# Kernel optimization log

Measured on AMD Instinct MI355X. Metric: run time of the kernel, lower is better.

The kernel has to match this reference:

```python
import jax, jax.numpy as jnp
import numpy as np
from math import sqrt

# dims
B, H, P, N, D = 4, 8, 32, 32, 16   # batch, heads, n_patches, channels, patch_len
L = P * N                           # 1024 token positions
SEQ, PRED, WIN, E, NF = 512, 96, 10, 2, 6  # seq_len, pred_len, attention_window, e_layers, n_fore
EPS = float(np.finfo(np.float32).eps)      # torch RMSNorm default eps (finfo eps)


def setup_inputs() -> dict:
    key = jax.random.key(0)
    ks = jax.random.split(key, 8)
    return dict(
        tokens=jax.random.normal(ks[0], (B, H, L, D), jnp.float32),
        x_original=jax.random.normal(ks[1], (B, SEQ, N), jnp.float32),
        log_scales=jnp.full((E,), np.log(2.0), jnp.float32),
        attn_norm_w=jnp.ones((E, D), jnp.float32),
        conv_up_w=jax.random.normal(ks[2], (E, 2 * H, 1, 3), jnp.float32) * 0.1,
        conv_down_w=jax.random.normal(ks[3], (E, H, 2, 1), jnp.float32) * 0.1,
        ffn_norm_w=jnp.ones((E, D), jnp.float32),
        mix_w=jax.random.normal(ks[4], (1, H), jnp.float32) * 0.3,
        mix_b=jnp.zeros((1,), jnp.float32),
        fore_w=jax.random.normal(ks[5], (NF, P), jnp.float32) * 0.1,
        fore_b=jnp.zeros((NF,), jnp.float32),
    )


def _rms(x, w):
    # torch.nn.RMSNorm over last dim (patch_len)
    return x * jax.lax.rsqrt(jnp.mean(x * x, axis=-1, keepdims=True) + EPS) * w


def _mask():
    # pid repeated per-channel; True entries are masked out
    pid = jnp.repeat(jnp.arange(P), N)
    diff = pid[None, :] - pid[:, None]  # pid[key] - pid[query]
    return (diff <= 0) | (diff >= WIN)  # [L, L]


def _signed_attn(h, log_scale, mask):
    # scores: [B,H,L,L]; A = softmax(+s) - softmax(-s) with banded mask
    scores = jnp.einsum('bhld,bhmd->bhlm', h, h)
    scale = jnp.clip(jnp.exp(log_scale), 1.0, 30.0) / sqrt(D)
    pos = jnp.where(mask, -10000.0, scores)
    neg = jnp.where(mask, -10000.0, -scores)
    A = jax.nn.softmax(scale * pos, axis=-1) - jax.nn.softmax(scale * neg, axis=-1)
    return jnp.einsum('bhlm,bhmd->bhld', A, h)


def _conv_ffn(x, up_w, down_w, norm_w):
    # depthwise causal conv along patch time dim D; x: [B,H,L,D]
    r = x.transpose(0, 2, 1, 3).reshape(B * L, H, D)
    r = jnp.pad(r, ((0, 0), (0, 0), (2, 0)))  # causal left-pad (kernel_size-1)
    dn = ('NCH', 'OIH', 'NCH')
    r = jax.lax.conv_general_dilated(r, up_w, (1,), 'VALID', dimension_numbers=dn, feature_group_count=H)
    r = jax.nn.gelu(r, approximate=False)
    r = jax.lax.conv_general_dilated(r, down_w, (1,), 'VALID', dimension_numbers=dn, feature_group_count=H)
    r = r.reshape(B, L, H, D).transpose(0, 2, 1, 3)
    return _rms(x + r, norm_w)


def reference(tokens, x_original, log_scales, attn_norm_w, conv_up_w, conv_down_w,
              ffn_norm_w, mix_w, mix_b, fore_w, fore_b):
    mask = _mask()
    h = tokens
    for l in range(E):
        h = _rms(h + _signed_attn(h, log_scales[l], mask), attn_norm_w[l])
        h = _conv_ffn(h, conv_up_w[l], conv_down_w[l], ffn_norm_w[l])
    # aggregate heads -> forecast
    h = h.reshape(B, H, P, N, D).transpose(0, 3, 4, 2, 1)       # (B,N,D,P,H)
    h = jnp.einsum('bndph,h->bndp', h, mix_w[0]) + mix_b[0]      # channel_mixing
    f = jnp.einsum('bndp,fp->bndf', h, fore_w) + fore_b          # fore_projection
    f = f.reshape(B, N, D * NF)[:, :, -PRED:]                    # flatten + tail slice
    forecast = f.transpose(0, 2, 1)                              # (B,pred_len,N)
    return forecast, x_original
```

## Files before the change

kernel.cpp:

```cpp
#include <hip/hip_runtime.h>
#include <hip/hip_bf16.h>
#include <math.h>

#define BB 4
#define HH 8
#define PP 32
#define NN 32
#define DD 16
#define LL 1024
#define WINW 10
#define NFF 6
#define PREDL 96
#define SEQL 512
#define EPSF 1.1920928955078125e-07f
#define KROW 24
#define KTS 296
#define PROW 40
#define XROW 20

typedef __attribute__((ext_vector_type(8))) short bf16x8;
typedef __attribute__((ext_vector_type(4))) float f32x4;

__device__ __forceinline__ unsigned cvtpk(float a, float b) {
    unsigned r;
    asm("v_cvt_pk_bf16_f32 %0, %1, %2" : "=v"(r) : "v"(a), "v"(b));
    return r;
}
__device__ __forceinline__ unsigned long long pk64(unsigned lo, unsigned hi) {
    return (unsigned long long)lo | ((unsigned long long)hi << 32);
}

template <int MODE>
__device__ __forceinline__ void layer_body(
    const float* __restrict__ hin, float* __restrict__ hout,
    const float* __restrict__ log_scales, const float* __restrict__ attn_norm,
    const float* __restrict__ up_w, const float* __restrict__ down_w,
    const float* __restrict__ ffn_norm, int layer, int blk, int tid,
    short* hK, short* VT, short (*Pp)[16 * PROW], short (*Pn)[16 * PROW],
    float* xls, float (*comb)[64][8], float (*combl)[2][16],
    const float* __restrict__ mix_w, const float* __restrict__ mix_b,
    const float* __restrict__ fore_w, const float* __restrict__ fore_b,
    float* __restrict__ out)
{
    int bh  = blk >> 5;
    int hh  = bh & 7;
    int p0  = blk & 31;
    int nstage = min(9, (PP - 1) - p0);

    int wid  = tid >> 6;
    int qh   = wid >> 1;
    int ch   = wid & 1;
    int lane = tid & 63;
    int quad = lane >> 4, n16 = lane & 15;

    {
        const float4* src = (const float4*)(hin + ((size_t)bh * LL + (p0 + 1) * NN) * DD);
        int nf4 = nstage * 128;
        #pragma unroll
        for (int k = 0; k < 5; ++k) {
            int i = tid + k * 256;
            if (i < nf4) {
                int row = i >> 2, j = i & 3;
                float4 v = src[i];
                unsigned pk0 = cvtpk(v.x, v.y);
                unsigned pk1 = cvtpk(v.z, v.w);
                *(unsigned long long*)&hK[row * KROW + j * 4] = pk64(pk0, pk1);
                int d0 = j * 4;
                VT[(d0 + 0) * KTS + row] = (short)(pk0 & 0xffff);
                VT[(d0 + 1) * KTS + row] = (short)(pk0 >> 16);
                VT[(d0 + 2) * KTS + row] = (short)(pk1 & 0xffff);
                VT[(d0 + 3) * KTS + row] = (short)(pk1 >> 16);
            }
        }
    }

    bf16x8 Aq;
    #pragma unroll
    for (int j = 0; j < 8; ++j) Aq[j] = 0;
    if (quad < 2) {
        const float4* qp4 = (const float4*)(hin +
            ((size_t)bh * LL + p0 * NN + qh * 16 + n16) * DD + quad * 8);
        float4 a = qp4[0], b = qp4[1];
        union { bf16x8 v; unsigned u[4]; } uu;
        uu.u[0] = cvtpk(a.x, a.y);
        uu.u[1] = cvtpk(a.z, a.w);
        uu.u[2] = cvtpk(b.x, b.y);
        uu.u[3] = cvtpk(b.z, b.w);
        Aq = uu.v;
    }
    float rs[4] = {0.f, 0.f, 0.f, 0.f};
    if (ch == 0) {
        #pragma unroll
        for (int r = 0; r < 4; ++r)
            rs[r] = hin[((size_t)bh * LL + p0 * NN + qh * 16 + quad * 4 + r) * DD + n16];
    }

    float sc  = fminf(fmaxf(__expf(log_scales[layer]), 1.0f), 30.0f) * 0.25f;
    float sc2 = sc * 1.4426950408889634f;

    __syncthreads();

    f32x4 Op, On;
    Op[0] = Op[1] = Op[2] = Op[3] = 0.f;
    On[0] = On[1] = On[2] = On[3] = 0.f;
    float lpp = 0.f, lnn = 0.f;
    short* myPp = Pp[wid];
    short* myPn = Pn[wid];

    int c0 = ch ? 4 : 0;
    int c1 = ch ? nstage : min(4, nstage);

    for (int c = c0; c < c1; ++c) {
        int kb = c * 32;
        #pragma unroll
        for (int kt = 0; kt < 2; ++kt) {
            bf16x8 Bk;
            #pragma unroll
            for (int j = 0; j < 8; ++j) Bk[j] = 0;
            if (quad < 2)
                Bk = *(const bf16x8*)&hK[(kb + kt * 16 + n16) * KROW + quad * 8];
            f32x4 z; z[0] = z[1] = z[2] = z[3] = 0.f;
            f32x4 S = __builtin_amdgcn_mfma_f32_16x16x32_bf16(Bk, Aq, z, 0, 0, 0);
            float ep[4], en[4];
            #pragma unroll
            for (int r = 0; r < 4; ++r) {
                float t = sc2 * S[r];
                ep[r] = exp2f(t);
                en[r] = exp2f(-t);
                lpp += ep[r]; lnn += en[r];
            }
            *(unsigned long long*)&myPp[n16 * PROW + kt * 16 + quad * 4] =
                pk64(cvtpk(ep[0], ep[1]), cvtpk(ep[2], ep[3]));
            *(unsigned long long*)&myPn[n16 * PROW + kt * 16 + quad * 4] =
                pk64(cvtpk(en[0], en[1]), cvtpk(en[2], en[3]));
        }
        bf16x8 Bv = *(const bf16x8*)&VT[n16 * KTS + kb + quad * 8];
        bf16x8 Ap = *(const bf16x8*)&myPp[n16 * PROW + quad * 8];
        bf16x8 An = *(const bf16x8*)&myPn[n16 * PROW + quad * 8];
        Op = __builtin_amdgcn_mfma_f32_16x16x32_bf16(Ap, Bv, Op, 0, 0, 0);
        On = __builtin_amdgcn_mfma_f32_16x16x32_bf16(An, Bv, On, 0, 0, 0);
    }

    lpp += __shfl_xor(lpp, 16); lpp += __shfl_xor(lpp, 32);
    lnn += __shfl_xor(lnn, 16); lnn += __shfl_xor(lnn, 32);

    if (ch == 1) {
        *(f32x4*)&comb[qh][lane][0] = Op;
        *(f32x4*)&comb[qh][lane][4] = On;
        if (lane < 16) {
            combl[qh][0][lane] = lpp;
            combl[qh][1][lane] = lnn;
        }
    }
    __syncthreads();
    if (ch == 1) return;

    {
        f32x4 o2 = *(const f32x4*)&comb[qh][lane][0];
        f32x4 n2 = *(const f32x4*)&comb[qh][lane][4];
        #pragma unroll
        for (int r = 0; r < 4; ++r) { Op[r] += o2[r]; On[r] += n2[r]; }
        lpp += combl[qh][0][n16];
        lnn += combl[qh][1][n16];
    }

    float lpr[4], lnr[4];
    #pragma unroll
    for (int r = 0; r < 4; ++r) {
        lpr[r] = __shfl(lpp, quad * 4 + r);
        lnr[r] = __shfl(lnn, quad * 4 + r);
    }

    #pragma unroll
    for (int r = 0; r < 4; ++r) {
        float lp = lpr[r], ln = lnr[r];
        float rl = (lp > 0.f) ? (1.0f / lp) : 0.f;
        float rn = (ln > 0.f) ? (1.0f / ln) : 0.f;
        float v  = rs[r] + Op[r] * rl - On[r] * rn;
        float ss = v * v;
        ss += __shfl_xor(ss, 1); ss += __shfl_xor(ss, 2);
        ss += __shfl_xor(ss, 4); ss += __shfl_xor(ss, 8);
        float rr = rsqrtf(ss * (1.0f / 16.0f) + EPSF);
        xls[(qh * 16 + quad * 4 + r) * XROW + n16] = v * rr * attn_norm[layer * DD + n16];
    }

    {
        int q = qh * 16 + n16;
        int g = quad;

        const float* uw = up_w + (size_t)(layer * 2 * HH + 2 * hh) * 3;
        float w00 = uw[0], w01 = uw[1], w02 = uw[2];
        float w10 = uw[3], w11 = uw[4], w12 = uw[5];
        const float* dw = down_w + (size_t)(layer * HH + hh) * 2;
        float dc0 = dw[0], dc1 = dw[1];

        float xm2 = g ? xls[q * XROW + 4 * g - 2] : 0.f;
        float xm1 = g ? xls[q * XROW + 4 * g - 1] : 0.f;
        float4 xv = *(const float4*)&xls[q * XROW + 4 * g];
        float xa[6] = {xm2, xm1, xv.x, xv.y, xv.z, xv.w};

        float v4[4], ss = 0.f;
        #pragma unroll
        for (int i = 0; i < 4; ++i) {
            float u0 = w00 * xa[i] + w01 * xa[i + 1] + w02 * xa[i + 2];
            float u1 = w10 * xa[i] + w11 * xa[i + 1] + w12 * xa[i + 2];
            float g0 = 0.5f * u0 * (1.0f + erff(u0 * 0.7071067811865475f));
            float g1 = 0.5f * u1 * (1.0f + erff(u1 * 0.7071067811865475f));
            float vv = xa[i] * 0.f + xa[i + 2] + dc0 * g0 + dc1 * g1;
            v4[i] = vv; ss += vv * vv;
        }
        ss += __shfl_xor(ss, 16); ss += __shfl_xor(ss, 32);
        float r2 = rsqrtf(ss * (1.0f / 16.0f) + EPSF);

        const float4 fn = *(const float4*)&ffn_norm[layer * DD + 4 * g];
        float vals[4];
        vals[0] = v4[0] * r2 * fn.x;
        vals[1] = v4[1] * r2 * fn.y;
        vals[2] = v4[2] * r2 * fn.z;
        vals[3] = v4[3] * r2 * fn.w;

        if (MODE == 0) {
            float* op = hout + ((size_t)bh * LL + p0 * NN + q) * DD + 4 * g;
            *(float4*)op = *(float4*)vals;
        } else {
            int b2 = bh >> 3;
            float mwh = mix_w[hh];
            bool isc = (hh == 0) && (p0 == 0);
            float mbv = mix_b[0];
            #pragma unroll
            for (int fi = 0; fi < NFF; ++fi) {
                float cst = 0.f;
                if (isc) {
                    float s = 0.f;
                    for (int p = 0; p < PP; ++p) s += fore_w[fi * PP + p];
                    cst = fore_b[fi] + mbv * s;
                }
                float c = mwh * fore_w[fi * PP + p0];
                #pragma unroll
                for (int i = 0; i < 4; ++i)
                    atomicAdd(&out[((size_t)(b2 * DD + 4 * g + i) * NFF + fi) * NN + q],
                              c * vals[i] + cst);
            }
        }
    }
}

__global__ __launch_bounds__(256) void layer0_kernel(
    const float* __restrict__ tokens, float* __restrict__ hA,
    const float* __restrict__ log_scales, const float* __restrict__ attn_norm,
    const float* __restrict__ up_w, const float* __restrict__ down_w,
    const float* __restrict__ ffn_norm,
    const float* __restrict__ x_orig, float* __restrict__ out)
{
    __shared__ short hK[9 * 32 * KROW];
    __shared__ short VT[16 * KTS];
    __shared__ short Pp[4][16 * PROW];
    __shared__ short Pn[4][16 * PROW];
    __shared__ float xls[32 * XROW];
    __shared__ float comb[2][64][8];
    __shared__ float combl[2][2][16];

    int blk = blockIdx.x;
    int tid = threadIdx.x;

    if (tid < 3) {
        float4 z; z.x = z.y = z.z = z.w = 0.f;
        ((float4*)out)[blk * 3 + tid] = z;
    }
    if (tid < 16) {
        const float4* x4 = (const float4*)x_orig;
        float4* o4 = (float4*)(out + BB * PREDL * NN);
        o4[blk * 16 + tid] = x4[blk * 16 + tid];
    }

    layer_body<0>(tokens, hA, log_scales, attn_norm, up_w, down_w, ffn_norm, 0,
                  blk, tid, hK, VT, Pp, Pn, xls, comb, combl,
                  nullptr, nullptr, nullptr, nullptr, nullptr);
}

__global__ __launch_bounds__(256) void layer1_kernel(
    const float* __restrict__ hA,
    const float* __restrict__ log_scales, const float* __restrict__ attn_norm,
    const float* __restrict__ up_w, const float* __restrict__ down_w,
    const float* __restrict__ ffn_norm,
    const float* __restrict__ mix_w, const float* __restrict__ mix_b,
    const float* __restrict__ fore_w, const float* __restrict__ fore_b,
    float* __restrict__ out)
{
    __shared__ short hK[9 * 32 * KROW];
    __shared__ short VT[16 * KTS];
    __shared__ short Pp[4][16 * PROW];
    __shared__ short Pn[4][16 * PROW];
    __shared__ float xls[32 * XROW];
    __shared__ float comb[2][64][8];
    __shared__ float combl[2][2][16];

    int blk = blockIdx.x;
    int tid = threadIdx.x;

    layer_body<1>(hA, nullptr, log_scales, attn_norm, up_w, down_w, ffn_norm, 1,
                  blk, tid, hK, VT, Pp, Pn, xls, comb, combl,
                  mix_w, mix_b, fore_w, fore_b, out);
}

static int find_by_size(const int* s, int n, int want, int occurrence) {
    int seen = 0;
    for (int i = 0; i < n; ++i)
        if (s[i] == want) { if (seen == occurrence) return i; ++seen; }
    return -1;
}

extern "C" void kernel_launch(void* const* d_in, const int* in_sizes, int n_in,
                              void* d_out, int out_size, void* d_ws, size_t ws_size,
                              hipStream_t stream) {
    int it  = find_by_size(in_sizes, n_in, 524288, 0);
    int ix  = find_by_size(in_sizes, n_in, 65536, 0);
    int ils = find_by_size(in_sizes, n_in, 2, 0);
    int ian = find_by_size(in_sizes, n_in, 32, 0);
    int icu = find_by_size(in_sizes, n_in, 96, 0);
    int icd = find_by_size(in_sizes, n_in, 32, 1);
    int ifn = find_by_size(in_sizes, n_in, 32, 2);
    int imw = find_by_size(in_sizes, n_in, 8, 0);
    int imb = find_by_size(in_sizes, n_in, 1, 0);
    int ifw = find_by_size(in_sizes, n_in, 192, 0);
    int ifb = find_by_size(in_sizes, n_in, 6, 0);
    if (it < 0 || ix < 0 || ils < 0 || ian < 0 || icu < 0 || icd < 0 ||
        ifn < 0 || imw < 0 || imb < 0 || ifw < 0 || ifb < 0) {
        it = 0; ix = 1; ils = 2; ian = 3; icu = 4; icd = 5; ifn = 6;
        imw = 7; imb = 8; ifw = 9; ifb = 10;
    }

    const float* tokens     = (const float*)d_in[it];
    const float* x_orig     = (const float*)d_in[ix];
    const float* log_scales = (const float*)d_in[ils];
    const float* attn_norm  = (const float*)d_in[ian];
    const float* up_w       = (const float*)d_in[icu];
    const float* down_w     = (const float*)d_in[icd];
    const float* ffn_norm   = (const float*)d_in[ifn];
    const float* mix_w      = (const float*)d_in[imw];
    const float* mix_b      = (const float*)d_in[imb];
    const float* fore_w     = (const float*)d_in[ifw];
    const float* fore_b     = (const float*)d_in[ifb];
    float* out = (float*)d_out;

    float* hA = (float*)d_ws;

    layer0_kernel<<<1024, 256, 0, stream>>>(tokens, hA, log_scales, attn_norm,
                                            up_w, down_w, ffn_norm, x_orig, out);
    layer1_kernel<<<1024, 256, 0, stream>>>(hA, log_scales, attn_norm,
                                            up_w, down_w, ffn_norm,
                                            mix_w, mix_b, fore_w, fore_b, out);
}
```

Baseline: 109.7 us.

## Fuse both encoder layers into one kernel with halo recomputation in LDS

After: 120.0 us. 9.4% more time.

```diff
diff --git a/kernel.cpp b/kernel.cpp
--- a/kernel.cpp
+++ b/kernel.cpp
@@ -8,13 +8,13 @@
 #define NN 32
 #define DD 16
 #define LL 1024
-#define WINW 10
 #define NFF 6
 #define PREDL 96
 #define SEQL 512
 #define EPSF 1.1920928955078125e-07f
 #define KROW 24
-#define KTS 296
+#define KTS0 680
+#define H1ROW 20
 #define PROW 40
 #define XROW 20
 
@@ -30,277 +30,361 @@
     return (unsigned long long)lo | ((unsigned long long)hi << 32);
 }
 
-template <int MODE>
-__device__ __forceinline__ void layer_body(
-    const float* __restrict__ hin, float* __restrict__ hout,
-    const float* __restrict__ log_scales, const float* __restrict__ attn_norm,
-    const float* __restrict__ up_w, const float* __restrict__ down_w,
-    const float* __restrict__ ffn_norm, int layer, int blk, int tid,
-    short* hK, short* VT, short (*Pp)[16 * PROW], short (*Pn)[16 * PROW],
-    float* xls, float (*comb)[64][8], float (*combl)[2][16],
-    const float* __restrict__ mix_w, const float* __restrict__ mix_b,
-    const float* __restrict__ fore_w, const float* __restrict__ fore_b,
-    float* __restrict__ out)
+__global__ __launch_bounds__(256) void prep_kernel(float* __restrict__ out)
 {
-    int bh  = blk >> 5;
-    int hh  = bh & 7;
-    int p0  = blk & 31;
-    int nstage = min(9, (PP - 1) - p0);
-
-    int wid  = tid >> 6;
-    int qh   = wid >> 1;
-    int ch   = wid & 1;
-    int lane = tid & 63;
-    int quad = lane >> 4, n16 = lane & 15;
-
-    {
-        const float4* src = (const float4*)(hin + ((size_t)bh * LL + (p0 + 1) * NN) * DD);
-        int nf4 = nstage * 128;
-        #pragma unroll
-        for (int k = 0; k < 5; ++k) {
-            int i = tid + k * 256;
-            if (i < nf4) {
-                int row = i >> 2, j = i & 3;
-                float4 v = src[i];
-                unsigned pk0 = cvtpk(v.x, v.y);
-                unsigned pk1 = cvtpk(v.z, v.w);
-                *(unsigned long long*)&hK[row * KROW + j * 4] = pk64(pk0, pk1);
-                int d0 = j * 4;
-                VT[(d0 + 0) * KTS + row] = (short)(pk0 & 0xffff);
-                VT[(d0 + 1) * KTS + row] = (short)(pk0 >> 16);
-                VT[(d0 + 2) * KTS + row] = (short)(pk1 & 0xffff);
-                VT[(d0 + 3) * KTS + row] = (short)(pk1 >> 16);
-            }
-        }
-    }
-
-    bf16x8 Aq;
-    #pragma unroll
-    for (int j = 0; j < 8; ++j) Aq[j] = 0;
-    if (quad < 2) {
-        const float4* qp4 = (const float4*)(hin +
-            ((size_t)bh * LL + p0 * NN + qh * 16 + n16) * DD + quad * 8);
-        float4 a = qp4[0], b = qp4[1];
-        union { bf16x8 v; unsigned u[4]; } uu;
-        uu.u[0] = cvtpk(a.x, a.y);
-        uu.u[1] = cvtpk(a.z, a.w);
-        uu.u[2] = cvtpk(b.x, b.y);
-        uu.u[3] = cvtpk(b.z, b.w);
-        Aq = uu.v;
-    }
-    float rs[4] = {0.f, 0.f, 0.f, 0.f};
-    if (ch == 0) {
-        #pragma unroll
-        for (int r = 0; r < 4; ++r)
-            rs[r] = hin[((size_t)bh * LL + p0 * NN + qh * 16 + quad * 4 + r) * DD + n16];
-    }
-
-    float sc  = fminf(fmaxf(__expf(log_scales[layer]), 1.0f), 30.0f) * 0.25f;
-    float sc2 = sc * 1.4426950408889634f;
-
-    __syncthreads();
-
-    f32x4 Op, On;
-    Op[0] = Op[1] = Op[2] = Op[3] = 0.f;
-    On[0] = On[1] = On[2] = On[3] = 0.f;
-    float lpp = 0.f, lnn = 0.f;
-    short* myPp = Pp[wid];
-    short* myPn = Pn[wid];
-
-    int c0 = ch ? 4 : 0;
-    int c1 = ch ? nstage : min(4, nstage);
-
-    for (int c = c0; c < c1; ++c) {
-        int kb = c * 32;
-        #pragma unroll
-        for (int kt = 0; kt < 2; ++kt) {
-            bf16x8 Bk;
-            #pragma unroll
-            for (int j = 0; j < 8; ++j) Bk[j] = 0;
-            if (quad < 2)
-                Bk = *(const bf16x8*)&hK[(kb + kt * 16 + n16) * KROW + quad * 8];
-            f32x4 z; z[0] = z[1] = z[2] = z[3] = 0.f;
-            f32x4 S = __builtin_amdgcn_mfma_f32_16x16x32_bf16(Bk, Aq, z, 0, 0, 0);
-            float ep[4], en[4];
-            #pragma unroll
-            for (int r = 0; r < 4; ++r) {
-                float t = sc2 * S[r];
-                ep[r] = exp2f(t);
-                en[r] = exp2f(-t);
-                lpp += ep[r]; lnn += en[r];
-            }
-            *(unsigned long long*)&myPp[n16 * PROW + kt * 16 + quad * 4] =
-                pk64(cvtpk(ep[0], ep[1]), cvtpk(ep[2], ep[3]));
-            *(unsigned long long*)&myPn[n16 * PROW + kt * 16 + quad * 4] =
-                pk64(cvtpk(en[0], en[1]), cvtpk(en[2], en[3]));
-        }
-        bf16x8 Bv = *(const bf16x8*)&VT[n16 * KTS + kb + quad * 8];
-        bf16x8 Ap = *(const bf16x8*)&myPp[n16 * PROW + quad * 8];
-        bf16x8 An = *(const bf16x8*)&myPn[n16 * PROW + quad * 8];
-        Op = __builtin_amdgcn_mfma_f32_16x16x32_bf16(Ap, Bv, Op, 0, 0, 0);
-        On = __builtin_amdgcn_mfma_f32_16x16x32_bf16(An, Bv, On, 0, 0, 0);
-    }
-
-    lpp += __shfl_xor(lpp, 16); lpp += __shfl_xor(lpp, 32);
-    lnn += __shfl_xor(lnn, 16); lnn += __shfl_xor(lnn, 32);
-
-    if (ch == 1) {
-        *(f32x4*)&comb[qh][lane][0] = Op;
-        *(f32x4*)&comb[qh][lane][4] = On;
-        if (lane < 16) {
-            combl[qh][0][lane] = lpp;
-            combl[qh][1][lane] = lnn;
-        }
-    }
-    __syncthreads();
-    if (ch == 1) return;
-
-    {
-        f32x4 o2 = *(const f32x4*)&comb[qh][lane][0];
-        f32x4 n2 = *(const f32x4*)&comb[qh][lane][4];
-        #pragma unroll
-        for (int r = 0; r < 4; ++r) { Op[r] += o2[r]; On[r] += n2[r]; }
-        lpp += combl[qh][0][n16];
-        lnn += combl[qh][1][n16];
-    }
-
-    float lpr[4], lnr[4];
-    #pragma unroll
-    for (int r = 0; r < 4; ++r) {
-        lpr[r] = __shfl(lpp, quad * 4 + r);
-        lnr[r] = __shfl(lnn, quad * 4 + r);
-    }
-
-    #pragma unroll
-    for (int r = 0; r < 4; ++r) {
-        float lp = lpr[r], ln = lnr[r];
-        float rl = (lp > 0.f) ? (1.0f / lp) : 0.f;
-        float rn = (ln > 0.f) ? (1.0f / ln) : 0.f;
-        float v  = rs[r] + Op[r] * rl - On[r] * rn;
-        float ss = v * v;
-        ss += __shfl_xor(ss, 1); ss += __shfl_xor(ss, 2);
-        ss += __shfl_xor(ss, 4); ss += __shfl_xor(ss, 8);
-        float rr = rsqrtf(ss * (1.0f / 16.0f) + EPSF);
-        xls[(qh * 16 + quad * 4 + r) * XROW + n16] = v * rr * attn_norm[layer * DD + n16];
-    }
-
-    {
-        int q = qh * 16 + n16;
-        int g = quad;
-
-        const float* uw = up_w + (size_t)(layer * 2 * HH + 2 * hh) * 3;
-        float w00 = uw[0], w01 = uw[1], w02 = uw[2];
-        float w10 = uw[3], w11 = uw[4], w12 = uw[5];
-        const float* dw = down_w + (size_t)(layer * HH + hh) * 2;
-        float dc0 = dw[0], dc1 = dw[1];
-
-        float xm2 = g ? xls[q * XROW + 4 * g - 2] : 0.f;
-        float xm1 = g ? xls[q * XROW + 4 * g - 1] : 0.f;
-        float4 xv = *(const float4*)&xls[q * XROW + 4 * g];
-        float xa[6] = {xm2, xm1, xv.x, xv.y, xv.z, xv.w};
-
-        float v4[4], ss = 0.f;
-        #pragma unroll
-        for (int i = 0; i < 4; ++i) {
-            float u0 = w00 * xa[i] + w01 * xa[i + 1] + w02 * xa[i + 2];
-            float u1 = w10 * xa[i] + w11 * xa[i + 1] + w12 * xa[i + 2];
-            float g0 = 0.5f * u0 * (1.0f + erff(u0 * 0.7071067811865475f));
-            float g1 = 0.5f * u1 * (1.0f + erff(u1 * 0.7071067811865475f));
-            float vv = xa[i] * 0.f + xa[i + 2] + dc0 * g0 + dc1 * g1;
-            v4[i] = vv; ss += vv * vv;
-        }
-        ss += __shfl_xor(ss, 16); ss += __shfl_xor(ss, 32);
-        float r2 = rsqrtf(ss * (1.0f / 16.0f) + EPSF);
-
-        const float4 fn = *(const float4*)&ffn_norm[layer * DD + 4 * g];
-        float vals[4];
-        vals[0] = v4[0] * r2 * fn.x;
-        vals[1] = v4[1] * r2 * fn.y;
-        vals[2] = v4[2] * r2 * fn.z;
-        vals[3] = v4[3] * r2 * fn.w;
-
-        if (MODE == 0) {
-            float* op = hout + ((size_t)bh * LL + p0 * NN + q) * DD + 4 * g;
-            *(float4*)op = *(float4*)vals;
-        } else {
-            int b2 = bh >> 3;
-            float mwh = mix_w[hh];
-            bool isc = (hh == 0) && (p0 == 0);
-            float mbv = mix_b[0];
-            #pragma unroll
-            for (int fi = 0; fi < NFF; ++fi) {
-                float cst = 0.f;
-                if (isc) {
-                    float s = 0.f;
-                    for (int p = 0; p < PP; ++p) s += fore_w[fi * PP + p];
-                    cst = fore_b[fi] + mbv * s;
-                }
-                float c = mwh * fore_w[fi * PP + p0];
-                #pragma unroll
-                for (int i = 0; i < 4; ++i)
-                    atomicAdd(&out[((size_t)(b2 * DD + 4 * g + i) * NFF + fi) * NN + q],
-                              c * vals[i] + cst);
-            }
-        }
-    }
-}
-
-__global__ __launch_bounds__(256) void layer0_kernel(
-    const float* __restrict__ tokens, float* __restrict__ hA,
-    const float* __restrict__ log_scales, const float* __restrict__ attn_norm,
-    const float* __restrict__ up_w, const float* __restrict__ down_w,
-    const float* __restrict__ ffn_norm,
-    const float* __restrict__ x_orig, float* __restrict__ out)
-{
-    __shared__ short hK[9 * 32 * KROW];
-    __shared__ short VT[16 * KTS];
-    __shared__ short Pp[4][16 * PROW];
-    __shared__ short Pn[4][16 * PROW];
-    __shared__ float xls[32 * XROW];
-    __shared__ float comb[2][64][8];
-    __shared__ float combl[2][2][16];
-
-    int blk = blockIdx.x;
-    int tid = threadIdx.x;
-
-    if (tid < 3) {
+    int t = blockIdx.x * 256 + threadIdx.x;
+    if (t < BB * DD * NFF * NN / 4) {
         float4 z; z.x = z.y = z.z = z.w = 0.f;
-        ((float4*)out)[blk * 3 + tid] = z;
-    }
-    if (tid < 16) {
-        const float4* x4 = (const float4*)x_orig;
-        float4* o4 = (float4*)(out + BB * PREDL * NN);
-        o4[blk * 16 + tid] = x4[blk * 16 + tid];
-    }
-
-    layer_body<0>(tokens, hA, log_scales, attn_norm, up_w, down_w, ffn_norm, 0,
-                  blk, tid, hK, VT, Pp, Pn, xls, comb, combl,
-                  nullptr, nullptr, nullptr, nullptr, nullptr);
-}
-
-__global__ __launch_bounds__(256) void layer1_kernel(
-    const float* __restrict__ hA,
+        ((float4*)out)[t] = z;
+    }
+}
+
+__global__ __launch_bounds__(512) void mega_kernel(
+    const float* __restrict__ tokens,
     const float* __restrict__ log_scales, const float* __restrict__ attn_norm,
     const float* __restrict__ up_w, const float* __restrict__ down_w,
     const float* __restrict__ ffn_norm,
     const float* __restrict__ mix_w, const float* __restrict__ mix_b,
     const float* __restrict__ fore_w, const float* __restrict__ fore_b,
-    float* __restrict__ out)
+    const float* __restrict__ x_orig, float* __restrict__ out)
 {
-    __shared__ short hK[9 * 32 * KROW];
-    __shared__ short VT[16 * KTS];
-    __shared__ short Pp[4][16 * PROW];
-    __shared__ short Pn[4][16 * PROW];
-    __shared__ float xls[32 * XROW];
-    __shared__ float comb[2][64][8];
-    __shared__ float combl[2][2][16];
+    __shared__ short hK0[672 * KROW];
+    __shared__ short VT0[16 * KTS0];
+    __shared__ float h1[13 * 32 * H1ROW];
+    __shared__ short Pp[8][16 * PROW];
+    __shared__ short Pn[8][16 * PROW];
+    __shared__ float xls[8][16 * XROW];
 
     int blk = blockIdx.x;
-    int tid = threadIdx.x;
-
-    layer_body<1>(hA, nullptr, log_scales, attn_norm, up_w, down_w, ffn_norm, 1,
-                  blk, tid, hK, VT, Pp, Pn, xls, comb, combl,
-                  mix_w, mix_b, fore_w, fore_b, out);
+    int bh  = blk >> 3;
+    int hh  = bh & 7;
+    int ri  = blk & 7;
+    int a   = ri * 4;
+    int lo0 = a;
+    int hi0 = min(32, a + 13);
+    int P0  = hi0 - lo0;
+    int klo = lo0 + 1;
+    int khi = min(32, hi0 + 9);
+    int KP0 = khi - klo;
+
+    int tid  = threadIdx.x;
+    int wid  = tid >> 6;
+    int lane = tid & 63;
+    int quad = lane >> 4, n16 = lane & 15;
+
+    if (tid < 64) {
+        const float4* x4 = (const float4*)x_orig;
+        float4* o4 = (float4*)(out + BB * PREDL * NN);
+        o4[blk * 64 + tid] = x4[blk * 64 + tid];
+    }
+
+    {
+        const float4* src = (const float4*)(tokens + ((size_t)bh * LL + klo * NN) * DD);
+        int nf4 = KP0 * 128;
+        for (int i = tid; i < nf4; i += 512) {
+            int row = i >> 2, j = i & 3;
+            float4 v = src[i];
+            unsigned pk0 = cvtpk(v.x, v.y);
+            unsigned pk1 = cvtpk(v.z, v.w);
+            *(unsigned long long*)&hK0[row * KROW + j * 4] = pk64(pk0, pk1);
+            int d0 = j * 4;
+            VT0[(d0 + 0) * KTS0 + row] = (short)(pk0 & 0xffff);
+            VT0[(d0 + 1) * KTS0 + row] = (short)(pk0 >> 16);
+            VT0[(d0 + 2) * KTS0 + row] = (short)(pk1 & 0xffff);
+            VT0[(d0 + 3) * KTS0 + row] = (short)(pk1 >> 16);
+        }
+    }
+
+    float sc0 = fminf(fmaxf(__expf(log_scales[0]), 1.0f), 30.0f)
+                * 0.25f * 1.4426950408889634f;
+    float sc1 = fminf(fmaxf(__expf(log_scales[1]), 1.0f), 30.0f)
+                * 0.25f * 1.4426950408889634f;
+
+    short* myPp = Pp[wid];
+    short* myPn = Pn[wid];
+    float* myxls = xls[wid];
+
+    __syncthreads();
+
+    {
+        int ntask = P0 * 2;
+        for (int t = wid; t < ntask; t += 8) {
+            int pi = t >> 1, qh = t & 1;
+            int p  = lo0 + pi;
+            int nst = min(9, 31 - p);
+
+            bf16x8 Aq;
+            #pragma unroll
+            for (int j = 0; j < 8; ++j) Aq[j] = 0;
+            if (quad < 2) {
+                const float4* qp4 = (const float4*)(tokens +
+                    ((size_t)bh * LL + p * NN + qh * 16 + n16) * DD + quad * 8);
+                float4 A = qp4[0], B = qp4[1];
+                union { bf16x8 v; unsigned u[4]; } uu;
+                uu.u[0] = cvtpk(A.x, A.y); uu.u[1] = cvtpk(A.z, A.w);
+                uu.u[2] = cvtpk(B.x, B.y); uu.u[3] = cvtpk(B.z, B.w);
+                Aq = uu.v;
+            }
+            float rs[4];
+            #pragma unroll
+            for (int r = 0; r < 4; ++r)
+                rs[r] = tokens[((size_t)bh * LL + p * NN + qh * 16 + quad * 4 + r) * DD + n16];
+
+            f32x4 Op, On;
+            Op[0] = Op[1] = Op[2] = Op[3] = 0.f;
+            On[0] = On[1] = On[2] = On[3] = 0.f;
+            float lpp = 0.f, lnn = 0.f;
+
+            for (int c = 0; c < nst; ++c) {
+                int kb = (p + 1 + c - klo) * 32;
+                #pragma unroll
+                for (int kt = 0; kt < 2; ++kt) {
+                    bf16x8 Bk;
+                    #pragma unroll
+                    for (int j = 0; j < 8; ++j) Bk[j] = 0;
+                    if (quad < 2)
+                        Bk = *(const bf16x8*)&hK0[(kb + kt * 16 + n16) * KROW + quad * 8];
+                    f32x4 z; z[0] = z[1] = z[2] = z[3] = 0.f;
+                    f32x4 S = __builtin_amdgcn_mfma_f32_16x16x32_bf16(Bk, Aq, z, 0, 0, 0);
+                    float ep[4], en[4];
+                    #pragma unroll
+                    for (int r = 0; r < 4; ++r) {
+                        float tt = sc0 * S[r];
+                        ep[r] = exp2f(tt);
+                        en[r] = exp2f(-tt);
+                        lpp += ep[r]; lnn += en[r];
+                    }
+                    *(unsigned long long*)&myPp[n16 * PROW + kt * 16 + quad * 4] =
+                        pk64(cvtpk(ep[0], ep[1]), cvtpk(ep[2], ep[3]));
+                    *(unsigned long long*)&myPn[n16 * PROW + kt * 16 + quad * 4] =
+                        pk64(cvtpk(en[0], en[1]), cvtpk(en[2], en[3]));
+                }
+                bf16x8 Bv = *(const bf16x8*)&VT0[n16 * KTS0 + kb + quad * 8];
+                bf16x8 Ap = *(const bf16x8*)&myPp[n16 * PROW + quad * 8];
+                bf16x8 An = *(const bf16x8*)&myPn[n16 * PROW + quad * 8];
+                Op = __builtin_amdgcn_mfma_f32_16x16x32_bf16(Ap, Bv, Op, 0, 0, 0);
+                On = __builtin_amdgcn_mfma_f32_16x16x32_bf16(An, Bv, On, 0, 0, 0);
+            }
+
+            lpp += __shfl_xor(lpp, 16); lpp += __shfl_xor(lpp, 32);
+            lnn += __shfl_xor(lnn, 16); lnn += __shfl_xor(lnn, 32);
+            float lpr[4], lnr[4];
+            #pragma unroll
+            for (int r = 0; r < 4; ++r) {
+                lpr[r] = __shfl(lpp, quad * 4 + r);
+                lnr[r] = __shfl(lnn, quad * 4 + r);
+            }
+
+            #pragma unroll
+            for (int r = 0; r < 4; ++r) {
+                float lp = lpr[r], ln = lnr[r];
+                float rl = (lp > 0.f) ? (1.0f / lp) : 0.f;
+                float rn = (ln > 0.f) ? (1.0f / ln) : 0.f;
+                float v  = rs[r] + Op[r] * rl - On[r] * rn;
+                float ss = v * v;
+                ss += __shfl_xor(ss, 1); ss += __shfl_xor(ss, 2);
+                ss += __shfl_xor(ss, 4); ss += __shfl_xor(ss, 8);
+                float rr = rsqrtf(ss * (1.0f / 16.0f) + EPSF);
+                myxls[(quad * 4 + r) * XROW + n16] = v * rr * attn_norm[0 * DD + n16];
+            }
+
+            {
+                int q = n16;
+                int g = quad;
+
+                const float* uw = up_w + (size_t)(0 * 2 * HH + 2 * hh) * 3;
+                float w00 = uw[0], w01 = uw[1], w02 = uw[2];
+                float w10 = uw[3], w11 = uw[4], w12 = uw[5];
+                const float* dw = down_w + (size_t)(0 * HH + hh) * 2;
+                float dc0 = dw[0], dc1 = dw[1];
+
+                float xm2 = g ? myxls[q * XROW + 4 * g - 2] : 0.f;
+                float xm1 = g ? myxls[q * XROW + 4 * g - 1] : 0.f;
+                float4 xv = *(const float4*)&myxls[q * XROW + 4 * g];
+                float xa[6] = {xm2, xm1, xv.x, xv.y, xv.z, xv.w};
+
+                float v4[4], ss = 0.f;
+                #pragma unroll
+                for (int i = 0; i < 4; ++i) {
+                    float u0 = w00 * xa[i] + w01 * xa[i + 1] + w02 * xa[i + 2];
+                    float u1 = w10 * xa[i] + w11 * xa[i + 1] + w12 * xa[i + 2];
+                    float g0 = 0.5f * u0 * (1.0f + erff(u0 * 0.7071067811865475f));
+                    float g1 = 0.5f * u1 * (1.0f + erff(u1 * 0.7071067811865475f));
+                    float vv = xa[i + 2] + dc0 * g0 + dc1 * g1;
+                    v4[i] = vv; ss += vv * vv;
+                }
+                ss += __shfl_xor(ss, 16); ss += __shfl_xor(ss, 32);
+                float r2 = rsqrtf(ss * (1.0f / 16.0f) + EPSF);
+
+                const float4 fn = *(const float4*)&ffn_norm[0 * DD + 4 * g];
+                float4 o;
+                o.x = v4[0] * r2 * fn.x;
+                o.y = v4[1] * r2 * fn.y;
+                o.z = v4[2] * r2 * fn.z;
+                o.w = v4[3] * r2 * fn.w;
+                *(float4*)&h1[(pi * 32 + qh * 16 + q) * H1ROW + 4 * g] = o;
+            }
+        }
+    }
+
+    __syncthreads();
+
+    {
+        int pi1 = wid >> 1, qh = wid & 1;
+        int p   = a + pi1;
+        int nst = min(9, 31 - p);
+
+        bf16x8 Aq;
+        #pragma unroll
+        for (int j = 0; j < 8; ++j) Aq[j] = 0;
+        if (quad < 2) {
+            const float* qp = &h1[(pi1 * 32 + qh * 16 + n16) * H1ROW + quad * 8];
+            float4 A = *(const float4*)qp;
+            float4 B = *(const float4*)(qp + 4);
+            union { bf16x8 v; unsigned u[4]; } uu;
+            uu.u[0] = cvtpk(A.x, A.y); uu.u[1] = cvtpk(A.z, A.w);
+            uu.u[2] = cvtpk(B.x, B.y); uu.u[3] = cvtpk(B.z, B.w);
+            Aq = uu.v;
+        }
+        float rs[4];
+        #pragma unroll
+        for (int r = 0; r < 4; ++r)
+            rs[r] = h1[(pi1 * 32 + qh * 16 + quad * 4 + r) * H1ROW + n16];
+
+        f32x4 Op, On;
+        Op[0] = Op[1] = Op[2] = Op[3] = 0.f;
+        On[0] = On[1] = On[2] = On[3] = 0.f;
+        float lpp = 0.f, lnn = 0.f;
+
+        for (int c = 0; c < nst; ++c) {
+            int kb = (pi1 + 1 + c) * 32;
+            #pragma unroll
+            for (int kt = 0; kt < 2; ++kt) {
+                bf16x8 Bk;
+                #pragma unroll
+                for (int j = 0; j < 8; ++j) Bk[j] = 0;
+                if (quad < 2) {
+                    const float* kp_ = &h1[(kb + kt * 16 + n16) * H1ROW + quad * 8];
+                    float4 A = *(const float4*)kp_;
+                    float4 B = *(const float4*)(kp_ + 4);
+                    union { bf16x8 v; unsigned u[4]; } uu;
+                    uu.u[0] = cvtpk(A.x, A.y); uu.u[1] = cvtpk(A.z, A.w);
+                    uu.u[2] = cvtpk(B.x, B.y); uu.u[3] = cvtpk(B.z, B.w);
+                    Bk = uu.v;
+                }
+                f32x4 z; z[0] = z[1] = z[2] = z[3] = 0.f;
+                f32x4 S = __builtin_amdgcn_mfma_f32_16x16x32_bf16(Bk, Aq, z, 0, 0, 0);
+                float ep[4], en[4];
+                #pragma unroll
+                for (int r = 0; r < 4; ++r) {
+                    float tt = sc1 * S[r];
+                    ep[r] = exp2f(tt);
+                    en[r] = exp2f(-tt);
+                    lpp += ep[r]; lnn += en[r];
+                }
+                *(unsigned long long*)&myPp[n16 * PROW + kt * 16 + quad * 4] =
+                    pk64(cvtpk(ep[0], ep[1]), cvtpk(ep[2], ep[3]));
+                *(unsigned long long*)&myPn[n16 * PROW + kt * 16 + quad * 4] =
+                    pk64(cvtpk(en[0], en[1]), cvtpk(en[2], en[3]));
+            }
+            bf16x8 Bv;
+            {
+                float v0 = h1[(kb + quad * 8 + 0) * H1ROW + n16];
+                float v1 = h1[(kb + quad * 8 + 1) * H1ROW + n16];
+                float v2 = h1[(kb + quad * 8 + 2) * H1ROW + n16];
+                float v3 = h1[(kb + quad * 8 + 3) * H1ROW + n16];
+                float v4_ = h1[(kb + quad * 8 + 4) * H1ROW + n16];
+                float v5 = h1[(kb + quad * 8 + 5) * H1ROW + n16];
+                float v6 = h1[(kb + quad * 8 + 6) * H1ROW + n16];
+                float v7 = h1[(kb + quad * 8 + 7) * H1ROW + n16];
+                union { bf16x8 v; unsigned u[4]; } uu;
+                uu.u[0] = cvtpk(v0, v1); uu.u[1] = cvtpk(v2, v3);
+                uu.u[2] = cvtpk(v4_, v5); uu.u[3] = cvtpk(v6, v7);
+                Bv = uu.v;
+            }
+            bf16x8 Ap = *(const bf16x8*)&myPp[n16 * PROW + quad * 8];
+            bf16x8 An = *(const bf16x8*)&myPn[n16 * PROW + quad * 8];
+            Op = __builtin_amdgcn_mfma_f32_16x16x32_bf16(Ap, Bv, Op, 0, 0, 0);
+            On = __builtin_amdgcn_mfma_f32_16x16x32_bf16(An, Bv, On, 0, 0, 0);
+        }
+
+        lpp += __shfl_xor(lpp, 16); lpp += __shfl_xor(lpp, 32);
+        lnn += __shfl_xor(lnn, 16); lnn += __shfl_xor(lnn, 32);
+        float lpr[4], lnr[4];
+        #pragma unroll
+        for (int r = 0; r < 4; ++r) {
+            lpr[r] = __shfl(lpp, quad * 4 + r);
+            lnr[r] = __shfl(lnn, quad * 4 + r);
+        }
+
+        #pragma unroll
+        for (int r = 0; r < 4; ++r) {
+            float lp = lpr[r], ln = lnr[r];
+            float rl = (lp > 0.f) ? (1.0f / lp) : 0.f;
+            float rn = (ln > 0.f) ? (1.0f / ln) : 0.f;
+            float v  = rs[r] + Op[r] * rl - On[r] * rn;
+            float ss = v * v;
+            ss += __shfl_xor(ss, 1); ss += __shfl_xor(ss, 2);
+            ss += __shfl_xor(ss, 4); ss += __shfl_xor(ss, 8);
+            float rr = rsqrtf(ss * (1.0f / 16.0f) + EPSF);
+            myxls[(quad * 4 + r) * XROW + n16] = v * rr * attn_norm[1 * DD + n16];
+        }
+
+        {
+            int q = qh * 16 + n16;
+            int g = quad;
+
+            const float* uw = up_w + (size_t)(1 * 2 * HH + 2 * hh) * 3;
+            float w00 = uw[0], w01 = uw[1], w02 = uw[2];
+            float w10 = uw[3], w11 = uw[4], w12 = uw[5];
+            const float* dw = down_w + (size_t)(1 * HH + hh) * 2;
+            float dc0 = dw[0], dc1 = dw[1];
+
+            float xm2 = g ? myxls[n16 * XROW + 4 * g - 2] : 0.f;
+            float xm1 = g ? myxls[n16 * XROW + 4 * g - 1] : 0.f;
+            float4 xv = *(const float4*)&myxls[n16 * XROW + 4 * g];
+            float xa[6] = {xm2, xm1, xv.x, xv.y, xv.z, xv.w};
+
+            float v4[4], ss = 0.f;
+            #pragma unroll
+            for (int i = 0; i < 4; ++i) {
+                float u0 = w00 * xa[i] + w01 * xa[i + 1] + w02 * xa[i + 2];
+                float u1 = w10 * xa[i] + w11 * xa[i + 1] + w12 * xa[i + 2];
+                float g0 = 0.5f * u0 * (1.0f + erff(u0 * 0.7071067811865475f));
+                float g1 = 0.5f * u1 * (1.0f + erff(u1 * 0.7071067811865475f));
+                float vv = xa[i + 2] + dc0 * g0 + dc1 * g1;
+                v4[i] = vv; ss += vv * vv;
+            }
+            ss += __shfl_xor(ss, 16); ss += __shfl_xor(ss, 32);
+            float r2 = rsqrtf(ss * (1.0f / 16.0f) + EPSF);
+
+            const float4 fn = *(const float4*)&ffn_norm[1 * DD + 4 * g];
+            float vals[4];
+            vals[0] = v4[0] * r2 * fn.x;
+            vals[1] = v4[1] * r2 * fn.y;
+            vals[2] = v4[2] * r2 * fn.z;
+            vals[3] = v4[3] * r2 * fn.w;
+
+            int b2 = bh >> 3;
+            float mwh = mix_w[hh];
+            bool isc = (hh == 0) && (p == 0);
+            float mbv = mix_b[0];
+            #pragma unroll
+            for (int fi = 0; fi < NFF; ++fi) {
+                float cst = 0.f;
+                if (isc) {
+                    float s = 0.f;
+                    for (int pp = 0; pp < PP; ++pp) s += fore_w[fi * PP + pp];
+                    cst = fore_b[fi] + mbv * s;
+                }
+                float cc = mwh * fore_w[fi * PP + p];
+                #pragma unroll
+                for (int i = 0; i < 4; ++i)
+                    atomicAdd(&out[((size_t)(b2 * DD + 4 * g + i) * NFF + fi) * NN + q],
+                              cc * vals[i] + cst);
+            }
+        }
+    }
 }
 
 static int find_by_size(const int* s, int n, int want, int occurrence) {
@@ -343,11 +427,9 @@
     const float* fore_b     = (const float*)d_in[ifb];
     float* out = (float*)d_out;
 
-    float* hA = (float*)d_ws;
-
-    layer0_kernel<<<1024, 256, 0, stream>>>(tokens, hA, log_scales, attn_norm,
-                                            up_w, down_w, ffn_norm, x_orig, out);
-    layer1_kernel<<<1024, 256, 0, stream>>>(hA, log_scales, attn_norm,
-                                            up_w, down_w, ffn_norm,
-                                            mix_w, mix_b, fore_w, fore_b, out);
-}
+    prep_kernel<<<12, 256, 0, stream>>>(out);
+    mega_kernel<<<256, 512, 0, stream>>>(tokens, log_scales, attn_norm,
+                                         up_w, down_w, ffn_norm,
+                                         mix_w, mix_b, fore_w, fore_b,
+                                         x_orig, out);
+}
```
